# Optimization experiments

Hardware: AMD Instinct MI355X
Metric: run time of the kernel (lower is better)

The kernel has to match this reference:

```python
import jax, jax.numpy as jnp
import numpy as np

B, C, H, W = 16, 384, 64, 64
NUM_POS = 48        # (7*7 - 1) offsets, origin excluded
STRIDE = 16
K = 3               # LO_kernel_size
SIGMA = 0.5         # LO_sigma


def setup_inputs() -> dict:
    key = jax.random.key(0)
    k1, k2 = jax.random.split(key)
    inp = jax.random.normal(k1, (B, C, H, W), dtype=jnp.float32)
    # init_offset: grid (iw*stride, ih*stride), skipping origin (use_origin=False)
    offs = []
    for ih in range(-3, 4):
        for iw in range(-3, 4):
            if ih == 0 and iw == 0:
                continue
            offs.append((iw * STRIDE, ih * STRIDE))
    offset = jnp.asarray(np.array(offs, dtype=np.float32))
    # small fractional perturbation so the learnable-offset gaussian path is non-trivial
    offset = offset + jax.random.uniform(k2, (NUM_POS, 2), minval=-0.45, maxval=0.45)
    return {"inp": inp, "offset": offset}


def _displace(inp, shift):
    """Integer per-channel-group spatial shift with zero padding.
    out[b,g,c,y,x] = inp[b,g,c, y - oy[g], x - ox[g]] (content moves by +offset).
    shift: [G,2] int32, (x, y) order as in the torch module.
    """
    b, c, h, w = inp.shape
    g = shift.shape[0]
    cpp = c // g
    x5 = inp.reshape(b, g, cpp, h, w)
    ox, oy = shift[:, 0], shift[:, 1]
    ys = jnp.arange(h, dtype=jnp.int32)[None, :] - oy[:, None]   # [G,H]
    xs = jnp.arange(w, dtype=jnp.int32)[None, :] - ox[:, None]   # [G,W]
    ymask = (ys >= 0) & (ys < h)
    xmask = (xs >= 0) & (xs < w)
    ysc = jnp.clip(ys, 0, h - 1)
    xsc = jnp.clip(xs, 0, w - 1)
    gth = jnp.take_along_axis(x5, ysc[None, :, None, :, None], axis=3)
    gth = jnp.take_along_axis(gth, xsc[None, :, None, None, :], axis=4)
    mask = (ymask[None, :, None, :, None] & xmask[None, :, None, None, :]).astype(inp.dtype)
    return (gth * mask).reshape(b, c, h, w)


def reference(inp, offset):
    b, c, h, w = inp.shape
    g = offset.shape[0]
    cpp = c // g
    # DisplaceCUDA uses offset.detach().round(): integer shift, no grad through it
    rnd = jax.lax.stop_gradient(jnp.round(offset))
    out = _displace(inp, rnd.astype(jnp.int32))
    # gaussian_translate: depthwise conv with gaussian kernel centered at
    # fractional part (offset - round(offset)); grads flow through this path only.
    frac = offset - rnd                                  # [G,2]
    r = jnp.arange(K, dtype=inp.dtype) - (K // 2)
    dx = r[None, None, :] + frac[:, 0, None, None]       # x varies along kernel width
    dy = r[None, :, None] + frac[:, 1, None, None]       # y varies along kernel height
    kern = jnp.exp(-(dx * dx + dy * dy) / (2.0 * SIGMA ** 2))   # [G,K,K]
    kern = kern / jnp.sum(kern, axis=(1, 2), keepdims=True)
    kern_full = jnp.repeat(kern, cpp, axis=0)[:, None]   # [C,1,K,K]
    out_LO = jax.lax.conv_general_dilated(
        out, kern_full, window_strides=(1, 1),
        padding=[(K // 2, K // 2), (K // 2, K // 2)],
        dimension_numbers=("NCHW", "OIHW", "NCHW"),
        feature_group_count=c)
    return out, out_LO
```

## Files before the change

kernel.cpp:

```cpp
#include <hip/hip_runtime.h>

#define B_   16
#define C_   384
#define H_   64
#define W_   64
#define PLANE (H_ * W_)
#define SCOLS 67
#define SROWS 66

__global__ __launch_bounds__(256) void displace_fused_kernel(
    const float* __restrict__ inp,
    const float* __restrict__ offset,
    float* __restrict__ out0,
    float* __restrict__ out1)
{
    __shared__ float s[SROWS * SCOLS];

    const int tid = threadIdx.x;
    const int p   = blockIdx.x;
    const int g   = (p % C_) >> 3;

    const float ofx = offset[2 * g + 0];
    const float ofy = offset[2 * g + 1];
    const float rx = rintf(ofx);
    const float ry = rintf(ofy);
    const float fx = ofx - rx;
    const float fy = ofy - ry;
    const int ox = (int)rx;
    const int oy = (int)ry;

    float w[9];
    {
        float sum = 0.0f;
        #pragma unroll
        for (int i = 0; i < 3; ++i) {
            const float dy = (float)(i - 1) + fy;
            #pragma unroll
            for (int j = 0; j < 3; ++j) {
                const float dx = (float)(j - 1) + fx;
                const float v = __expf(-(dx * dx + dy * dy) * 2.0f);
                w[i * 3 + j] = v;
                sum += v;
            }
        }
        const float inv = 1.0f / sum;
        #pragma unroll
        for (int k = 0; k < 9; ++k) w[k] *= inv;
    }

    if (tid < 67) { s[tid] = 0.0f; s[65 * SCOLS + tid] = 0.0f; }
    if (tid < 64) { s[(tid + 1) * SCOLS] = 0.0f; s[(tid + 1) * SCOLS + 65] = 0.0f; }

    const float* __restrict__ plane = inp + (size_t)p * PLANE;
    const int lane = tid & 63;
    const int wv   = tid >> 6;
    const int sx   = lane - ox;
    const bool vx  = (unsigned)sx < (unsigned)W_;

    float v[16];
    #pragma unroll
    for (int k = 0; k < 16; ++k) {
        const int y  = (k << 2) + wv;
        const int sy = y - oy;
        v[k] = (vx && (unsigned)sy < (unsigned)H_) ? plane[sy * W_ + sx] : 0.0f;
    }
    #pragma unroll
    for (int k = 0; k < 16; ++k) {
        const int y = (k << 2) + wv;
        s[(y + 1) * SCOLS + 1 + lane] = v[k];
    }
    __syncthreads();

    float* __restrict__ o0 = out0 + (size_t)p * PLANE;
    float* __restrict__ o1 = out1 + (size_t)p * PLANE;

    #pragma unroll
    for (int it = 0; it < 4; ++it) {
        const int base = it * 1024 + tid * 4;
        const int y = base >> 6;
        const int x = base & 63;
        const float* r0 = &s[y * SCOLS + x];
        const float* r1 = r0 + SCOLS;
        const float* r2 = r1 + SCOLS;

        float p0[6], p1[6], p2[6];
        #pragma unroll
        for (int j = 0; j < 6; ++j) { p0[j] = r0[j]; p1[j] = r1[j]; p2[j] = r2[j]; }

        const float4 d0 = make_float4(p1[1], p1[2], p1[3], p1[4]);

        float a0, a1, a2, a3;
        a0 = p0[0]*w[0] + p0[1]*w[1] + p0[2]*w[2]
           + p1[0]*w[3] + p1[1]*w[4] + p1[2]*w[5]
           + p2[0]*w[6] + p2[1]*w[7] + p2[2]*w[8];
        a1 = p0[1]*w[0] + p0[2]*w[1] + p0[3]*w[2]
           + p1[1]*w[3] + p1[2]*w[4] + p1[3]*w[5]
           + p2[1]*w[6] + p2[2]*w[7] + p2[3]*w[8];
        a2 = p0[2]*w[0] + p0[3]*w[1] + p0[4]*w[2]
           + p1[2]*w[3] + p1[3]*w[4] + p1[4]*w[5]
           + p2[2]*w[6] + p2[3]*w[7] + p2[4]*w[8];
        a3 = p0[3]*w[0] + p0[4]*w[1] + p0[5]*w[2]
           + p1[3]*w[3] + p1[4]*w[4] + p1[5]*w[5]
           + p2[3]*w[6] + p2[4]*w[7] + p2[5]*w[8];

        *(float4*)(o0 + base) = d0;
        *(float4*)(o1 + base) = make_float4(a0, a1, a2, a3);
    }
}

extern "C" void kernel_launch(void* const* d_in, const int* in_sizes, int n_in,
                              void* d_out, int out_size, void* d_ws, size_t ws_size,
                              hipStream_t stream) {
    const float* inp    = (const float*)d_in[0];
    const float* offset = (const float*)d_in[1];
    float* out0 = (float*)d_out;
    float* out1 = out0 + (size_t)B_ * C_ * PLANE;
    displace_fused_kernel<<<B_ * C_, 256, 0, stream>>>(inp, offset, out0, out1);
}
```

Before: 269.1 us.

## Process eight channel planes per block with double-buffered LDS prefetch

Each block now handles all 8 channels of one (batch, group) pair instead of a single plane, so the grid shrinks from 6144 to 768 blocks. The next plane's shifted global loads go into registers while the current plane is convolved out of one of two LDS buffers, and are written into the other buffer after the compute. The offset and Gaussian weight setup is also done once per group rather than once per plane. The aim is to hide global load latency behind compute, at the cost of far fewer resident blocks per CU and less parallelism overall.

```diff
diff --git a/kernel.cpp b/kernel.cpp
--- a/kernel.cpp
+++ b/kernel.cpp
@@ -4,21 +4,23 @@
 #define C_   384
 #define H_   64
 #define W_   64
+#define G_   48
 #define PLANE (H_ * W_)
 #define SCOLS 67
 #define SROWS 66
+#define SELEM (SROWS * SCOLS)
 
-__global__ __launch_bounds__(256) void displace_fused_kernel(
+__global__ __launch_bounds__(256) void displace_fused_pipe(
     const float* __restrict__ inp,
     const float* __restrict__ offset,
     float* __restrict__ out0,
     float* __restrict__ out1)
 {
-    __shared__ float s[SROWS * SCOLS];
+    __shared__ float s[2][SELEM];
 
     const int tid = threadIdx.x;
-    const int p   = blockIdx.x;
-    const int g   = (p % C_) >> 3;
+    const int g   = blockIdx.x % G_;
+    const int b   = blockIdx.x / G_;
 
     const float ofx = offset[2 * g + 0];
     const float ofy = offset[2 * g + 1];
@@ -48,63 +50,92 @@
         for (int k = 0; k < 9; ++k) w[k] *= inv;
     }
 
-    if (tid < 67) { s[tid] = 0.0f; s[65 * SCOLS + tid] = 0.0f; }
-    if (tid < 64) { s[(tid + 1) * SCOLS] = 0.0f; s[(tid + 1) * SCOLS + 65] = 0.0f; }
+    #pragma unroll
+    for (int bb = 0; bb < 2; ++bb) {
+        if (tid < 67) { s[bb][tid] = 0.0f; s[bb][65 * SCOLS + tid] = 0.0f; }
+        if (tid < 64) { s[bb][(tid + 1) * SCOLS] = 0.0f; s[bb][(tid + 1) * SCOLS + 65] = 0.0f; }
+    }
 
-    const float* __restrict__ plane = inp + (size_t)p * PLANE;
     const int lane = tid & 63;
     const int wv   = tid >> 6;
     const int sx   = lane - ox;
     const bool vx  = (unsigned)sx < (unsigned)W_;
+
+    const float* __restrict__ base = inp + ((size_t)b * C_ + (size_t)g * 8) * PLANE;
+    float* __restrict__ ob0 = out0 + ((size_t)b * C_ + (size_t)g * 8) * PLANE;
+    float* __restrict__ ob1 = out1 + ((size_t)b * C_ + (size_t)g * 8) * PLANE;
 
     float v[16];
     #pragma unroll
     for (int k = 0; k < 16; ++k) {
         const int y  = (k << 2) + wv;
         const int sy = y - oy;
-        v[k] = (vx && (unsigned)sy < (unsigned)H_) ? plane[sy * W_ + sx] : 0.0f;
+        v[k] = (vx && (unsigned)sy < (unsigned)H_) ? base[sy * W_ + sx] : 0.0f;
     }
     #pragma unroll
     for (int k = 0; k < 16; ++k) {
         const int y = (k << 2) + wv;
-        s[(y + 1) * SCOLS + 1 + lane] = v[k];
+        s[0][(y + 1) * SCOLS + 1 + lane] = v[k];
     }
     __syncthreads();
 
-    float* __restrict__ o0 = out0 + (size_t)p * PLANE;
-    float* __restrict__ o1 = out1 + (size_t)p * PLANE;
+    #pragma unroll
+    for (int i = 0; i < 8; ++i) {
+        if (i < 7) {
+            const float* __restrict__ plane = base + (size_t)(i + 1) * PLANE;
+            #pragma unroll
+            for (int k = 0; k < 16; ++k) {
+                const int y  = (k << 2) + wv;
+                const int sy = y - oy;
+                v[k] = (vx && (unsigned)sy < (unsigned)H_) ? plane[sy * W_ + sx] : 0.0f;
+            }
+        }
 
-    #pragma unroll
-    for (int it = 0; it < 4; ++it) {
-        const int base = it * 1024 + tid * 4;
-        const int y = base >> 6;
-        const int x = base & 63;
-        const float* r0 = &s[y * SCOLS + x];
-        const float* r1 = r0 + SCOLS;
-        const float* r2 = r1 + SCOLS;
+        const float* __restrict__ sb = s[i & 1];
+        float* __restrict__ o0 = ob0 + (size_t)i * PLANE;
+        float* __restrict__ o1 = ob1 + (size_t)i * PLANE;
+        #pragma unroll
+        for (int it = 0; it < 4; ++it) {
+            const int pbase = it * 1024 + tid * 4;
+            const int y = pbase >> 6;
+            const int x = pbase & 63;
+            const float* r0 = &sb[y * SCOLS + x];
+            const float* r1 = r0 + SCOLS;
+            const float* r2 = r1 + SCOLS;
 
-        float p0[6], p1[6], p2[6];
-        #pragma unroll
-        for (int j = 0; j < 6; ++j) { p0[j] = r0[j]; p1[j] = r1[j]; p2[j] = r2[j]; }
+            float p0[6], p1[6], p2[6];
+            #pragma unroll
+            for (int j = 0; j < 6; ++j) { p0[j] = r0[j]; p1[j] = r1[j]; p2[j] = r2[j]; }
 
-        const float4 d0 = make_float4(p1[1], p1[2], p1[3], p1[4]);
+            const float4 d0 = make_float4(p1[1], p1[2], p1[3], p1[4]);
 
-        float a0, a1, a2, a3;
-        a0 = p0[0]*w[0] + p0[1]*w[1] + p0[2]*w[2]
-           + p1[0]*w[3] + p1[1]*w[4] + p1[2]*w[5]
-           + p2[0]*w[6] + p2[1]*w[7] + p2[2]*w[8];
-        a1 = p0[1]*w[0] + p0[2]*w[1] + p0[3]*w[2]
-           + p1[1]*w[3] + p1[2]*w[4] + p1[3]*w[5]
-           + p2[1]*w[6] + p2[2]*w[7] + p2[3]*w[8];
-        a2 = p0[2]*w[0] + p0[3]*w[1] + p0[4]*w[2]
-           + p1[2]*w[3] + p1[3]*w[4] + p1[4]*w[5]
-           + p2[2]*w[6] + p2[3]*w[7] + p2[4]*w[8];
-        a3 = p0[3]*w[0] + p0[4]*w[1] + p0[5]*w[2]
-           + p1[3]*w[3] + p1[4]*w[4] + p1[5]*w[5]
-           + p2[3]*w[6] + p2[4]*w[7] + p2[5]*w[8];
+            float a0, a1, a2, a3;
+            a0 = p0[0]*w[0] + p0[1]*w[1] + p0[2]*w[2]
+               + p1[0]*w[3] + p1[1]*w[4] + p1[2]*w[5]
+               + p2[0]*w[6] + p2[1]*w[7] + p2[2]*w[8];
+            a1 = p0[1]*w[0] + p0[2]*w[1] + p0[3]*w[2]
+               + p1[1]*w[3] + p1[2]*w[4] + p1[3]*w[5]
+               + p2[1]*w[6] + p2[2]*w[7] + p2[3]*w[8];
+            a2 = p0[2]*w[0] + p0[3]*w[1] + p0[4]*w[2]
+               + p1[2]*w[3] + p1[3]*w[4] + p1[4]*w[5]
+               + p2[2]*w[6] + p2[3]*w[7] + p2[4]*w[8];
+            a3 = p0[3]*w[0] + p0[4]*w[1] + p0[5]*w[2]
+               + p1[3]*w[3] + p1[4]*w[4] + p1[5]*w[5]
+               + p2[3]*w[6] + p2[4]*w[7] + p2[5]*w[8];
 
-        *(float4*)(o0 + base) = d0;
-        *(float4*)(o1 + base) = make_float4(a0, a1, a2, a3);
+            *(float4*)(o0 + pbase) = d0;
+            *(float4*)(o1 + pbase) = make_float4(a0, a1, a2, a3);
+        }
+
+        if (i < 7) {
+            float* __restrict__ sw = s[(i + 1) & 1];
+            #pragma unroll
+            for (int k = 0; k < 16; ++k) {
+                const int y = (k << 2) + wv;
+                sw[(y + 1) * SCOLS + 1 + lane] = v[k];
+            }
+            __syncthreads();
+        }
     }
 }
 
@@ -115,5 +146,5 @@
     const float* offset = (const float*)d_in[1];
     float* out0 = (float*)d_out;
     float* out1 = out0 + (size_t)B_ * C_ * PLANE;
-    displace_fused_kernel<<<B_ * C_, 256, 0, stream>>>(inp, offset, out0, out1);
+    displace_fused_pipe<<<B_ * G_, 256, 0, stream>>>(inp, offset, out0, out1);
 }
```

New measurement: 273.5 us. No clear change (+1.6%).

## Use separable Gaussian with wavefront shuffles instead of shared-memory 3x3 stencil

Applied to the files above, without the earlier changes.

The 2D Gaussian kernel is factored into separate x and y 1D weights. The horizontal pass uses wavefront shuffles across the 64 lanes of a row. The vertical pass runs in registers, with each wave owning 16 rows plus a 2-row halo. This removes the shared-memory tile, its zero padding, the __syncthreads barrier and the LDS reads, and it cuts the FMA count. In exchange, stores become scalar (coalesced per row but not float4), and each wave reloads 2 halo rows from global memory.

```diff
diff --git a/kernel.cpp b/kernel.cpp
--- a/kernel.cpp
+++ b/kernel.cpp
@@ -4,18 +4,15 @@
 #define C_   384
 #define H_   64
 #define W_   64
+#define G_   48
 #define PLANE (H_ * W_)
-#define SCOLS 67
-#define SROWS 66
 
-__global__ __launch_bounds__(256) void displace_fused_kernel(
+__global__ __launch_bounds__(256) void displace_fused_shfl(
     const float* __restrict__ inp,
     const float* __restrict__ offset,
     float* __restrict__ out0,
     float* __restrict__ out1)
 {
-    __shared__ float s[SROWS * SCOLS];
-
     const int tid = threadIdx.x;
     const int p   = blockIdx.x;
     const int g   = (p % C_) >> 3;
@@ -29,82 +26,56 @@
     const int ox = (int)rx;
     const int oy = (int)ry;
 
-    float w[9];
+    float wx[3], wy[3];
     {
-        float sum = 0.0f;
+        float sxs = 0.0f, sys = 0.0f;
         #pragma unroll
-        for (int i = 0; i < 3; ++i) {
-            const float dy = (float)(i - 1) + fy;
-            #pragma unroll
-            for (int j = 0; j < 3; ++j) {
-                const float dx = (float)(j - 1) + fx;
-                const float v = __expf(-(dx * dx + dy * dy) * 2.0f);
-                w[i * 3 + j] = v;
-                sum += v;
-            }
+        for (int j = 0; j < 3; ++j) {
+            const float dx = (float)(j - 1) + fx;
+            const float dy = (float)(j - 1) + fy;
+            wx[j] = __expf(-dx * dx * 2.0f);
+            wy[j] = __expf(-dy * dy * 2.0f);
+            sxs += wx[j]; sys += wy[j];
         }
-        const float inv = 1.0f / sum;
+        const float ix = 1.0f / sxs, iy = 1.0f / sys;
         #pragma unroll
-        for (int k = 0; k < 9; ++k) w[k] *= inv;
+        for (int j = 0; j < 3; ++j) { wx[j] *= ix; wy[j] *= iy; }
     }
 
-    if (tid < 67) { s[tid] = 0.0f; s[65 * SCOLS + tid] = 0.0f; }
-    if (tid < 64) { s[(tid + 1) * SCOLS] = 0.0f; s[(tid + 1) * SCOLS + 65] = 0.0f; }
-
-    const float* __restrict__ plane = inp + (size_t)p * PLANE;
     const int lane = tid & 63;
     const int wv   = tid >> 6;
+    const int y0   = wv << 4;
     const int sx   = lane - ox;
     const bool vx  = (unsigned)sx < (unsigned)W_;
 
-    float v[16];
+    const float* __restrict__ plane = inp + (size_t)p * PLANE;
+
+    float v[18];
     #pragma unroll
-    for (int k = 0; k < 16; ++k) {
-        const int y  = (k << 2) + wv;
+    for (int k = 0; k < 18; ++k) {
+        const int y  = y0 - 1 + k;
         const int sy = y - oy;
-        v[k] = (vx && (unsigned)sy < (unsigned)H_) ? plane[sy * W_ + sx] : 0.0f;
+        v[k] = (vx && (unsigned)y < (unsigned)H_ && (unsigned)sy < (unsigned)H_)
+                 ? plane[sy * W_ + sx] : 0.0f;
     }
+
+    float Hh[18];
     #pragma unroll
-    for (int k = 0; k < 16; ++k) {
-        const int y = (k << 2) + wv;
-        s[(y + 1) * SCOLS + 1 + lane] = v[k];
+    for (int k = 0; k < 18; ++k) {
+        const float su = __shfl_up(v[k], 1, 64);
+        const float sd = __shfl_down(v[k], 1, 64);
+        const float L = (lane == 0)  ? 0.0f : su;
+        const float R = (lane == 63) ? 0.0f : sd;
+        Hh[k] = L * wx[0] + v[k] * wx[1] + R * wx[2];
     }
-    __syncthreads();
 
-    float* __restrict__ o0 = out0 + (size_t)p * PLANE;
-    float* __restrict__ o1 = out1 + (size_t)p * PLANE;
+    float* __restrict__ o0 = out0 + (size_t)p * PLANE + y0 * W_ + lane;
+    float* __restrict__ o1 = out1 + (size_t)p * PLANE + y0 * W_ + lane;
 
     #pragma unroll
-    for (int it = 0; it < 4; ++it) {
-        const int base = it * 1024 + tid * 4;
-        const int y = base >> 6;
-        const int x = base & 63;
-        const float* r0 = &s[y * SCOLS + x];
-        const float* r1 = r0 + SCOLS;
-        const float* r2 = r1 + SCOLS;
-
-        float p0[6], p1[6], p2[6];
-        #pragma unroll
-        for (int j = 0; j < 6; ++j) { p0[j] = r0[j]; p1[j] = r1[j]; p2[j] = r2[j]; }
-
-        const float4 d0 = make_float4(p1[1], p1[2], p1[3], p1[4]);
-
-        float a0, a1, a2, a3;
-        a0 = p0[0]*w[0] + p0[1]*w[1] + p0[2]*w[2]
-           + p1[0]*w[3] + p1[1]*w[4] + p1[2]*w[5]
-           + p2[0]*w[6] + p2[1]*w[7] + p2[2]*w[8];
-        a1 = p0[1]*w[0] + p0[2]*w[1] + p0[3]*w[2]
-           + p1[1]*w[3] + p1[2]*w[4] + p1[3]*w[5]
-           + p2[1]*w[6] + p2[2]*w[7] + p2[3]*w[8];
-        a2 = p0[2]*w[0] + p0[3]*w[1] + p0[4]*w[2]
-           + p1[2]*w[3] + p1[3]*w[4] + p1[4]*w[5]
-           + p2[2]*w[6] + p2[3]*w[7] + p2[4]*w[8];
-        a3 = p0[3]*w[0] + p0[4]*w[1] + p0[5]*w[2]
-           + p1[3]*w[3] + p1[4]*w[4] + p1[5]*w[5]
-           + p2[3]*w[6] + p2[4]*w[7] + p2[5]*w[8];
-
-        *(float4*)(o0 + base) = d0;
-        *(float4*)(o1 + base) = make_float4(a0, a1, a2, a3);
+    for (int r = 0; r < 16; ++r) {
+        o0[r * W_] = v[r + 1];
+        o1[r * W_] = Hh[r] * wy[0] + Hh[r + 1] * wy[1] + Hh[r + 2] * wy[2];
     }
 }
 
@@ -115,5 +86,5 @@
     const float* offset = (const float*)d_in[1];
     float* out0 = (float*)d_out;
     float* out1 = out0 + (size_t)B_ * C_ * PLANE;
-    displace_fused_kernel<<<B_ * C_, 256, 0, stream>>>(inp, offset, out0, out1);
+    displace_fused_shfl<<<B_ * C_, 256, 0, stream>>>(inp, offset, out0, out1);
 }
```

Result: no change. 266.8 us (-0.9%).
